# Performance work log

Hardware: AMD Instinct MI355X
Metric: run time of the kernel (lower is better)

Reference implementation:

```python
import jax, jax.numpy as jnp
import numpy as np

N, IN_DIM, OUT_DIM, HEADS = 8192, 256, 256, 2
C = OUT_DIM // HEADS  # per-head channel dim (concat=True)
ALPHA = 0.2
NEG = -9e15


def setup_inputs() -> dict:
    key = jax.random.key(0)
    ks = jax.random.split(key, 9)
    h = jax.random.normal(ks[0], (N, IN_DIM), dtype=jnp.float32)
    adj = jax.random.randint(ks[1], (N, N), 0, 2, dtype=jnp.int32)
    # torch nn.Linear weights are [out, in]; xavier-like scale
    def xav(k, shape):
        fan_in, fan_out = shape[1], shape[0]
        s = 1.414 * np.sqrt(6.0 / (fan_in + fan_out))
        return jax.random.uniform(k, shape, jnp.float32, -s, s)
    W1 = xav(ks[2], (HEADS * C, IN_DIM))
    W2 = xav(ks[3], (HEADS * C, IN_DIM))
    W3 = xav(ks[4], (HEADS * C, IN_DIM))
    b1 = jnp.zeros((HEADS * C,), jnp.float32)
    b2 = jnp.zeros((HEADS * C,), jnp.float32)
    b3 = jnp.zeros((HEADS * C,), jnp.float32)
    sa = 1.414 * np.sqrt(6.0 / (HEADS + 2 * C))
    a = jax.random.uniform(ks[5], (HEADS, 2 * C), jnp.float32, -sa, sa)
    return {"h": h, "adj": adj, "W1": W1, "b1": b1, "W2": W2, "b2": b2,
            "W3": W3, "b3": b3, "a": a}


def reference(h, adj, W1, b1, W2, b2, W3, b3, a):
    n = h.shape[0]
    W1h = (h @ W1.T + b1).reshape(n, HEADS, C)  # [N,H,C]
    W2h = (h @ W2.T + b2).reshape(n, HEADS, C)
    W3h = (h @ W3.T + b3).reshape(n, HEADS, C)
    # eij = a . [W1h_i || W2h_j] decomposes into per-node scores
    a1, a2 = a[:, :C], a[:, C:]
    s1 = jnp.einsum('nhc,hc->nh', W1h, a1)  # [N,H]
    s2 = jnp.einsum('nhc,hc->nh', W2h, a2)  # [N,H]
    e = jax.nn.leaky_relu(s1[:, None, :] + s2[None, :, :], ALPHA)  # [N,N,H]
    e = jnp.where(adj[:, :, None] == 1, e, NEG)
    att = jax.nn.softmax(e, axis=1)  # softmax over source dim j (dim=1)
    # dropout is identity in eval mode (training=False)
    h_prime = jnp.einsum('ijh,jhc->ihc', att, W3h)  # [N,H,C]
    return h_prime.reshape(n, HEADS * C)
```

## Files before the change

### kernel.cpp

```cpp
#include <hip/hip_runtime.h>
#include <hip/hip_bf16.h>

#define NN 8192
#define LOG2E 1.44269504088896f
#define S_SPLIT 8
#define JC 1024
#define NT 32

typedef __attribute__((ext_vector_type(8))) short short8;
typedef __attribute__((ext_vector_type(4))) float f32x4;
typedef __attribute__((ext_vector_type(4))) int int4v;

static __device__ __forceinline__ float bf2f(unsigned short u) {
    union { unsigned int i; float f; } v; v.i = ((unsigned int)u) << 16; return v.f;
}
static __device__ __forceinline__ unsigned short f2bf(float f) {
    union { float f; unsigned int i; } v; v.f = f;
    unsigned int lsb = (v.i >> 16) & 1u;
    v.i += 0x7fffu + lsb;
    return (unsigned short)(v.i >> 16);
}
static __device__ __forceinline__ unsigned int cvtpk(float lo, float hi) {
    unsigned int r;
    asm("v_cvt_pk_bf16_f32 %0, %1, %2" : "=v"(r) : "v"(lo), "v"(hi));
    return r;
}
static __device__ __forceinline__ float fexp2(float x) { return __builtin_amdgcn_exp2f(x); }

static __device__ __forceinline__ void cvt8(const float* __restrict__ p, short8& hi, short8& lo) {
    float4 u = *(const float4*)p;
    float4 v = *(const float4*)(p + 4);
    float f[8] = {u.x, u.y, u.z, u.w, v.x, v.y, v.z, v.w};
#pragma unroll
    for (int j = 0; j < 8; ++j) {
        unsigned short hb = f2bf(f[j]);
        hi[j] = (short)hb;
        lo[j] = (short)f2bf(f[j] - bf2f(hb));
    }
}

__global__ void prep_partial(const float* __restrict__ W1, const float* __restrict__ W2,
                             const float* __restrict__ a,
                             float* __restrict__ v1p, float* __restrict__ v2p) {
    int b = blockIdx.x;
    int t = threadIdx.x;
    int hh = t >> 8, k = t & 255;
    int c0 = (b & 7) * 16;
    const float* W = (b < 8) ? W1 : W2;
    int aoff = (b < 8) ? 0 : 128;
    float acc = 0.f;
    for (int c = c0; c < c0 + 16; ++c)
        acc += W[(size_t)(hh * 128 + c) * 256 + k] * a[hh * 256 + aoff + c];
    ((b < 8) ? v1p : v2p)[(b & 7) * 512 + t] = acc;
}

__global__ void prep_reduce(const float* __restrict__ b1, const float* __restrict__ b2,
                            const float* __restrict__ a,
                            const float* __restrict__ v1p, const float* __restrict__ v2p,
                            float* __restrict__ v1, float* __restrict__ v2, float* __restrict__ bd) {
    int t = threadIdx.x;
    float a1 = 0.f, a2 = 0.f;
    for (int b = 0; b < 8; ++b) { a1 += v1p[b * 512 + t]; a2 += v2p[b * 512 + t]; }
    v1[t] = a1;
    v2[t] = a2;
    int g = t >> 7;
    int hh = g >> 1, which = g & 1, c = t & 127;
    float prod = which ? b2[hh * 128 + c] * a[hh * 256 + 128 + c]
                       : b1[hh * 128 + c] * a[hh * 256 + c];
#pragma unroll
    for (int off = 1; off < 64; off <<= 1) prod += __shfl_xor(prod, off);
    __shared__ float ws[8];
    if ((t & 63) == 0) ws[t >> 6] = prod;
    __syncthreads();
    if (t < 4) bd[t] = ws[2 * t] + ws[2 * t + 1];
}

__global__ __launch_bounds__(256) void s_kernel(const float* __restrict__ hmat,
                         const float* __restrict__ v1, const float* __restrict__ v2,
                         const float* __restrict__ bd,
                         float* __restrict__ s1o, float* __restrict__ s2o) {
    int w = threadIdx.x >> 6, l = threadIdx.x & 63;
    int n = blockIdx.x * 4 + w;
    float4 hv  = *(const float4*)(hmat + (size_t)n * 256 + l * 4);
    float4 va0 = *(const float4*)(v1 + l * 4);
    float4 va1 = *(const float4*)(v1 + 256 + l * 4);
    float4 vb0 = *(const float4*)(v2 + l * 4);
    float4 vb1 = *(const float4*)(v2 + 256 + l * 4);
    float s10 = hv.x*va0.x + hv.y*va0.y + hv.z*va0.z + hv.w*va0.w;
    float s11 = hv.x*va1.x + hv.y*va1.y + hv.z*va1.z + hv.w*va1.w;
    float s20 = hv.x*vb0.x + hv.y*vb0.y + hv.z*vb0.z + hv.w*vb0.w;
    float s21 = hv.x*vb1.x + hv.y*vb1.y + hv.z*vb1.z + hv.w*vb1.w;
#pragma unroll
    for (int off = 1; off < 64; off <<= 1) {
        s10 += __shfl_xor(s10, off);
        s11 += __shfl_xor(s11, off);
        s20 += __shfl_xor(s20, off);
        s21 += __shfl_xor(s21, off);
    }
    if (l == 0) {
        s1o[n*2 + 0] = (s10 + bd[0]) * LOG2E;
        s1o[n*2 + 1] = (s11 + bd[2]) * LOG2E;
        s2o[n]       = (s20 + bd[1]) * LOG2E;
        s2o[NN + n]  = (s21 + bd[3]) * LOG2E;
    }
}

__global__ void wcvt_kernel(const float* __restrict__ W3,
                            unsigned short* __restrict__ w3hi, unsigned short* __restrict__ w3lo) {
    int i = blockIdx.x * 256 + threadIdx.x;
    float f = W3[i];
    unsigned short hb = f2bf(f);
    w3hi[i] = hb;
    w3lo[i] = f2bf(f - bf2f(hb));
}

__global__ __launch_bounds__(256) void w3_kernel(const float* __restrict__ hmat,
                                                 const unsigned short* __restrict__ w3hi,
                                                 const unsigned short* __restrict__ w3lo,
                                                 const float* __restrict__ b3,
                                                 unsigned short* __restrict__ w3b) {
    int tid = threadIdx.x;
    int w = tid >> 6, l = tid & 63;
    int m = l & 15, kq = l >> 4;
    int n0 = (blockIdx.x * 2 + (w & 1)) * 16;
    int c0 = (w >> 1) * 8;
    f32x4 acc[8];
#pragma unroll
    for (int ct = 0; ct < 8; ++ct) acc[ct] = (f32x4){0.f, 0.f, 0.f, 0.f};
    for (int k0 = 0; k0 < 256; k0 += 32) {
        short8 ahi, alo;
        cvt8(hmat + (size_t)(n0 + m) * 256 + k0 + kq * 8, ahi, alo);
#pragma unroll
        for (int ct = 0; ct < 8; ++ct) {
            int c = (c0 + ct) * 16 + m;
            short8 bhi = *(const short8*)&w3hi[(size_t)c * 256 + k0 + kq * 8];
            short8 blo = *(const short8*)&w3lo[(size_t)c * 256 + k0 + kq * 8];
            acc[ct] = __builtin_amdgcn_mfma_f32_16x16x32_bf16(ahi, bhi, acc[ct], 0, 0, 0);
            acc[ct] = __builtin_amdgcn_mfma_f32_16x16x32_bf16(alo, bhi, acc[ct], 0, 0, 0);
            acc[ct] = __builtin_amdgcn_mfma_f32_16x16x32_bf16(ahi, blo, acc[ct], 0, 0, 0);
        }
    }
#pragma unroll
    for (int ct = 0; ct < 8; ++ct) {
        int c = (c0 + ct) * 16 + m;
        float bias = b3[c];
#pragma unroll
        for (int e = 0; e < 4; ++e) {
            int n = n0 + kq * 4 + e;
            size_t idx = ((size_t)(n >> 5) * 16 + (c >> 4)) * 512 + (size_t)((((n >> 3) & 3) * 16 + m) * 8 + (n & 7));
            w3b[idx] = f2bf(acc[ct][e] + bias);
        }
    }
}

__global__ __launch_bounds__(512, 4) void attn_fused(
        const int* __restrict__ adj, const float* __restrict__ s1a,
        const float* __restrict__ s2h, const unsigned short* __restrict__ w3b,
        unsigned short* __restrict__ pacc, float* __restrict__ pden)
{
    __shared__ unsigned short Pt[2][2][64][32];
    __shared__ float s2t[2][JC];

    const int tid = threadIdx.x;
    const int wv = tid >> 6, ln = tid & 63;
    const int m = ln & 15, kq = ln >> 4;
    const int rg = wv & 1, cg = wv >> 1;
    const int hw = cg >> 1;
    const int r = tid >> 3, oct = tid & 7;
    const int i0 = blockIdx.x * 64;
    const int sidx = blockIdx.y;
    const int j0 = sidx * JC;
    const int sw = kq ^ ((m >> 1) & 3);

    const float s1r0 = s1a[(i0 + r) * 2 + 0];
    const float s1r1 = s1a[(i0 + r) * 2 + 1];
    const int* adjRow = adj + (size_t)(i0 + r) * NN + j0 + oct * 4;
    unsigned short* ptw = &Pt[0][0][0][0] + r * 32 + ((((oct >> 1) ^ ((r >> 1) & 3)) << 3) | ((oct & 1) << 2));
    const unsigned short* pta = &Pt[0][0][0][0] + (size_t)hw * 2048 + (rg * 32 + m) * 32 + (sw << 3);
    const unsigned short* w3p = w3b + ((size_t)(j0 >> 5) * 16 + cg * 4) * 512 + ln * 8;

    f32x4 acc[2][4];
    f32x4 accd[2];
#pragma unroll
    for (int rt = 0; rt < 2; ++rt) {
        accd[rt] = (f32x4){0.f, 0.f, 0.f, 0.f};
#pragma unroll
        for (int f = 0; f < 4; ++f) acc[rt][f] = (f32x4){0.f, 0.f, 0.f, 0.f};
    }
    short8 ones;
#pragma unroll
    for (int e = 0; e < 8; ++e) ones[e] = (short)0x3F80;

    for (int x = tid; x < 2 * JC; x += 512) {
        int h = x >> 10, j = x & (JC - 1);
        s2t[h][j] = s2h[(size_t)h * NN + j0 + j];
    }
    int4v aCur = __builtin_nontemporal_load((const int4v*)(adjRow));
    int4v aNxt = __builtin_nontemporal_load((const int4v*)(adjRow + 32));
    __syncthreads();

    for (int t = 0; t < NT; ++t) {
        const int buf = t & 1;
        const unsigned short* bp = w3p + (size_t)t * 8192;
        short8 bf0 = *(const short8*)(bp);
        short8 bf1 = *(const short8*)(bp + 512);
        short8 bf2 = *(const short8*)(bp + 1024);
        short8 bf3 = *(const short8*)(bp + 1536);
        int tn2 = (t + 2 < NT) ? t + 2 : NT - 1;
        int4v aNew = __builtin_nontemporal_load((const int4v*)(adjRow + tn2 * 32));
        {
            float4 sv0 = *(const float4*)&s2t[0][t * 32 + oct * 4];
            float4 sv1 = *(const float4*)&s2t[1][t * 32 + oct * 4];
            float x0, q0, q1, q2, q3, u0, u1, u2, u3;
            x0 = s1r0 + sv0.x; x0 = fmaxf(x0, 0.2f * x0); q0 = aCur.x ? fexp2(x0) : 0.f;
            x0 = s1r0 + sv0.y; x0 = fmaxf(x0, 0.2f * x0); q1 = aCur.y ? fexp2(x0) : 0.f;
            x0 = s1r0 + sv0.z; x0 = fmaxf(x0, 0.2f * x0); q2 = aCur.z ? fexp2(x0) : 0.f;
            x0 = s1r0 + sv0.w; x0 = fmaxf(x0, 0.2f * x0); q3 = aCur.w ? fexp2(x0) : 0.f;
            x0 = s1r1 + sv1.x; x0 = fmaxf(x0, 0.2f * x0); u0 = aCur.x ? fexp2(x0) : 0.f;
            x0 = s1r1 + sv1.y; x0 = fmaxf(x0, 0.2f * x0); u1 = aCur.y ? fexp2(x0) : 0.f;
            x0 = s1r1 + sv1.z; x0 = fmaxf(x0, 0.2f * x0); u2 = aCur.z ? fexp2(x0) : 0.f;
            x0 = s1r1 + sv1.w; x0 = fmaxf(x0, 0.2f * x0); u3 = aCur.w ? fexp2(x0) : 0.f;
            uint2 w0 = {cvtpk(q0, q1), cvtpk(q2, q3)};
            uint2 w1 = {cvtpk(u0, u1), cvtpk(u2, u3)};
            unsigned short* pw = ptw + buf * 4096;
            *(uint2*)pw = w0;
            *(uint2*)(pw + 2048) = w1;
        }
        asm volatile("s_waitcnt lgkmcnt(0)" ::: "memory");
        __builtin_amdgcn_sched_barrier(0);
        __builtin_amdgcn_s_barrier();
        asm volatile("" ::: "memory");
        {
            const unsigned short* pa = pta + buf * 4096;
            short8 a0 = *(const short8*)pa;
            short8 a1 = *(const short8*)(pa + 512);
            __builtin_amdgcn_s_setprio(1);
            acc[0][0] = __builtin_amdgcn_mfma_f32_16x16x32_bf16(a0, bf0, acc[0][0], 0, 0, 0);
            acc[1][0] = __builtin_amdgcn_mfma_f32_16x16x32_bf16(a1, bf0, acc[1][0], 0, 0, 0);
            acc[0][1] = __builtin_amdgcn_mfma_f32_16x16x32_bf16(a0, bf1, acc[0][1], 0, 0, 0);
            acc[1][1] = __builtin_amdgcn_mfma_f32_16x16x32_bf16(a1, bf1, acc[1][1], 0, 0, 0);
            acc[0][2] = __builtin_amdgcn_mfma_f32_16x16x32_bf16(a0, bf2, acc[0][2], 0, 0, 0);
            acc[1][2] = __builtin_amdgcn_mfma_f32_16x16x32_bf16(a1, bf2, acc[1][2], 0, 0, 0);
            acc[0][3] = __builtin_amdgcn_mfma_f32_16x16x32_bf16(a0, bf3, acc[0][3], 0, 0, 0);
            acc[1][3] = __builtin_amdgcn_mfma_f32_16x16x32_bf16(a1, bf3, acc[1][3], 0, 0, 0);
            if ((cg & 1) == 0) {
                accd[0] = __builtin_amdgcn_mfma_f32_16x16x32_bf16(a0, ones, accd[0], 0, 0, 0);
                accd[1] = __builtin_amdgcn_mfma_f32_16x16x32_bf16(a1, ones, accd[1], 0, 0, 0);
            }
            __builtin_amdgcn_s_setprio(0);
        }
        aCur = aNxt; aNxt = aNew;
    }

    if ((cg & 1) == 0 && m == 0) {
#pragma unroll
        for (int rt = 0; rt < 2; ++rt)
#pragma unroll
            for (int e = 0; e < 4; ++e) {
                int row = i0 + rg * 32 + rt * 16 + kq * 4 + e;
                pden[((size_t)sidx * NN + row) * 2 + hw] = accd[rt][e];
            }
    }
    size_t pb_ = (size_t)sidx * NN * 256;
#pragma unroll
    for (int rt = 0; rt < 2; ++rt)
#pragma unroll
        for (int e = 0; e < 4; ++e) {
            int row = i0 + rg * 32 + rt * 16 + kq * 4 + e;
#pragma unroll
            for (int f = 0; f < 4; ++f) {
                int col = cg * 64 + f * 16 + m;
                __builtin_nontemporal_store(f2bf(acc[rt][f][e]), &pacc[pb_ + (size_t)row * 256 + col]);
            }
        }
}

__global__ void combine_kernel(const unsigned short* __restrict__ pacc, const float* __restrict__ pden,
                               float* __restrict__ out) {
    size_t idx = ((size_t)blockIdx.x * 256 + threadIdx.x) * 8;
    int i = (int)(idx >> 8);
    int c = (int)(idx & 255);
    int hh = c >> 7;
    float acc[8];
#pragma unroll
    for (int e = 0; e < 8; ++e) acc[e] = 0.f;
    float den = 0.f;
    for (int s = 0; s < S_SPLIT; ++s) {
        uint4 v = *(const uint4*)&pacc[(size_t)s * NN * 256 + idx];
        unsigned int uu[4] = {v.x, v.y, v.z, v.w};
#pragma unroll
        for (int q = 0; q < 4; ++q) {
            acc[2*q]   += bf2f((unsigned short)(uu[q] & 0xffff));
            acc[2*q+1] += bf2f((unsigned short)(uu[q] >> 16));
        }
        den += pden[((size_t)s * NN + i) * 2 + hh];
    }
    float r = 1.f / den;
    float4 o0 = {acc[0]*r, acc[1]*r, acc[2]*r, acc[3]*r};
    float4 o1 = {acc[4]*r, acc[5]*r, acc[6]*r, acc[7]*r};
    *(float4*)&out[idx] = o0;
    *(float4*)&out[idx + 4] = o1;
}

extern "C" void kernel_launch(void* const* d_in, const int* in_sizes, int n_in,
                              void* d_out, int out_size, void* d_ws, size_t ws_size,
                              hipStream_t stream) {
    const float* hmat = (const float*)d_in[0];
    const int*   adj  = (const int*)d_in[1];
    const float* W1   = (const float*)d_in[2];
    const float* b1   = (const float*)d_in[3];
    const float* W2   = (const float*)d_in[4];
    const float* b2   = (const float*)d_in[5];
    const float* W3   = (const float*)d_in[6];
    const float* b3   = (const float*)d_in[7];
    const float* a    = (const float*)d_in[8];
    float* out = (float*)d_out;

    char* p = (char*)d_ws;
    float* v1   = (float*)p; p += 2048;
    float* v2   = (float*)p; p += 2048;
    float* bd   = (float*)p; p += 256;
    float* s1   = (float*)p; p += (size_t)NN * 2 * sizeof(float);
    float* s2h  = (float*)p; p += (size_t)NN * 2 * sizeof(float);
    float* v1p  = (float*)p; p += 8 * 512 * sizeof(float);
    float* v2p  = (float*)p; p += 8 * 512 * sizeof(float);
    unsigned short* w3hi = (unsigned short*)p; p += 65536 * 2;
    unsigned short* w3lo = (unsigned short*)p; p += 65536 * 2;
    unsigned short* w3b  = (unsigned short*)p; p += (size_t)NN * 256 * 2;
    float* pden = (float*)p; p += (size_t)S_SPLIT * NN * 2 * sizeof(float);
    unsigned short* pacc = (unsigned short*)p;

    prep_partial<<<16, 512, 0, stream>>>(W1, W2, a, v1p, v2p);
    prep_reduce<<<1, 512, 0, stream>>>(b1, b2, a, v1p, v2p, v1, v2, bd);
    s_kernel<<<NN / 4, 256, 0, stream>>>(hmat, v1, v2, bd, s1, s2h);
    wcvt_kernel<<<256, 256, 0, stream>>>(W3, w3hi, w3lo);
    w3_kernel<<<256, 256, 0, stream>>>(hmat, w3hi, w3lo, b3, w3b);
    attn_fused<<<dim3(NN / 64, S_SPLIT), 512, 0, stream>>>(adj, s1, s2h, w3b, pacc, pden);
    combine_kernel<<<(NN * 256) / (256 * 8), 256, 0, stream>>>(pacc, pden, out);
}
```

Measured before the change: 172.1 us.

## Pre-pack adjacency into bitmask and restructure attention to 256 threads

Adds a pre-pass that compresses the int32 adjacency matrix into one bit per entry. The attention kernel then stages these bits in shared memory instead of streaming int32 rows. The attention kernel drops to 4 waves per block, each computing all 64 rows, so it issues twice the MFMAs per wave with more accumulator registers. The softmax denominator moves from ones-vector MFMAs to scalar sums reduced with shuffles. Adjacency still has to be read in full once by the pack kernel, so the total traffic saving is small and an extra launch is added.

```diff
diff --git a/kernel.cpp b/kernel.cpp
--- a/kernel.cpp
+++ b/kernel.cpp
@@ -9,7 +9,6 @@
 
 typedef __attribute__((ext_vector_type(8))) short short8;
 typedef __attribute__((ext_vector_type(4))) float f32x4;
-typedef __attribute__((ext_vector_type(4))) int int4v;
 
 static __device__ __forceinline__ float bf2f(unsigned short u) {
     union { unsigned int i; float f; } v; v.i = ((unsigned int)u) << 16; return v.f;
@@ -37,6 +36,22 @@
         hi[j] = (short)hb;
         lo[j] = (short)f2bf(f[j] - bf2f(hb));
     }
+}
+
+__global__ __launch_bounds__(256) void pack_kernel(const int* __restrict__ adj,
+                                                   unsigned int* __restrict__ abits) {
+    int w = blockIdx.x * 256 + threadIdx.x;
+    const int* src = adj + (size_t)w * 32;
+    unsigned int bits = 0;
+#pragma unroll
+    for (int k = 0; k < 8; ++k) {
+        int4 v = *(const int4*)(src + k * 4);
+        bits |= (unsigned int)(v.x & 1) << (k * 4 + 0);
+        bits |= (unsigned int)(v.y & 1) << (k * 4 + 1);
+        bits |= (unsigned int)(v.z & 1) << (k * 4 + 2);
+        bits |= (unsigned int)(v.w & 1) << (k * 4 + 3);
+    }
+    abits[w] = bits;
 }
 
 __global__ void prep_partial(const float* __restrict__ W1, const float* __restrict__ W2,
@@ -153,20 +168,21 @@
     }
 }
 
-__global__ __launch_bounds__(512, 4) void attn_fused(
-        const int* __restrict__ adj, const float* __restrict__ s1a,
+__global__ __launch_bounds__(256, 4) void attn_fused(
+        const unsigned int* __restrict__ abits, const float* __restrict__ s1a,
         const float* __restrict__ s2h, const unsigned short* __restrict__ w3b,
         unsigned short* __restrict__ pacc, float* __restrict__ pden)
 {
     __shared__ unsigned short Pt[2][2][64][32];
     __shared__ float s2t[2][JC];
+    __shared__ unsigned int abt[64][32];
 
     const int tid = threadIdx.x;
-    const int wv = tid >> 6, ln = tid & 63;
+    const int ln = tid & 63;
     const int m = ln & 15, kq = ln >> 4;
-    const int rg = wv & 1, cg = wv >> 1;
+    const int cg = tid >> 6;
     const int hw = cg >> 1;
-    const int r = tid >> 3, oct = tid & 7;
+    const int r = tid >> 2, oc = tid & 3;
     const int i0 = blockIdx.x * 64;
     const int sidx = blockIdx.y;
     const int j0 = sidx * JC;
@@ -174,29 +190,25 @@
 
     const float s1r0 = s1a[(i0 + r) * 2 + 0];
     const float s1r1 = s1a[(i0 + r) * 2 + 1];
-    const int* adjRow = adj + (size_t)(i0 + r) * NN + j0 + oct * 4;
-    unsigned short* ptw = &Pt[0][0][0][0] + r * 32 + ((((oct >> 1) ^ ((r >> 1) & 3)) << 3) | ((oct & 1) << 2));
-    const unsigned short* pta = &Pt[0][0][0][0] + (size_t)hw * 2048 + (rg * 32 + m) * 32 + (sw << 3);
+    unsigned short* ptw = &Pt[0][0][0][0] + r * 32 + ((oc ^ ((r >> 1) & 3)) << 3);
+    const unsigned short* pta = &Pt[0][0][0][0] + hw * 2048 + m * 32 + (sw << 3);
     const unsigned short* w3p = w3b + ((size_t)(j0 >> 5) * 16 + cg * 4) * 512 + ln * 8;
 
-    f32x4 acc[2][4];
-    f32x4 accd[2];
-#pragma unroll
-    for (int rt = 0; rt < 2; ++rt) {
-        accd[rt] = (f32x4){0.f, 0.f, 0.f, 0.f};
+    f32x4 acc[4][4];
+#pragma unroll
+    for (int rt = 0; rt < 4; ++rt)
 #pragma unroll
         for (int f = 0; f < 4; ++f) acc[rt][f] = (f32x4){0.f, 0.f, 0.f, 0.f};
-    }
-    short8 ones;
-#pragma unroll
-    for (int e = 0; e < 8; ++e) ones[e] = (short)0x3F80;
-
-    for (int x = tid; x < 2 * JC; x += 512) {
+    float d0 = 0.f, d1 = 0.f;
+
+    for (int x = tid; x < 2 * JC; x += 256) {
         int h = x >> 10, j = x & (JC - 1);
         s2t[h][j] = s2h[(size_t)h * NN + j0 + j];
     }
-    int4v aCur = __builtin_nontemporal_load((const int4v*)(adjRow));
-    int4v aNxt = __builtin_nontemporal_load((const int4v*)(adjRow + 32));
+    for (int x = tid; x < 64 * 32; x += 256) {
+        int rr = x >> 5, tt = x & 31;
+        abt[rr][tt] = abits[(size_t)(i0 + rr) * 256 + (j0 >> 5) + tt];
+    }
     __syncthreads();
 
     for (int t = 0; t < NT; ++t) {
@@ -206,25 +218,30 @@
         short8 bf1 = *(const short8*)(bp + 512);
         short8 bf2 = *(const short8*)(bp + 1024);
         short8 bf3 = *(const short8*)(bp + 1536);
-        int tn2 = (t + 2 < NT) ? t + 2 : NT - 1;
-        int4v aNew = __builtin_nontemporal_load((const int4v*)(adjRow + tn2 * 32));
         {
-            float4 sv0 = *(const float4*)&s2t[0][t * 32 + oct * 4];
-            float4 sv1 = *(const float4*)&s2t[1][t * 32 + oct * 4];
-            float x0, q0, q1, q2, q3, u0, u1, u2, u3;
-            x0 = s1r0 + sv0.x; x0 = fmaxf(x0, 0.2f * x0); q0 = aCur.x ? fexp2(x0) : 0.f;
-            x0 = s1r0 + sv0.y; x0 = fmaxf(x0, 0.2f * x0); q1 = aCur.y ? fexp2(x0) : 0.f;
-            x0 = s1r0 + sv0.z; x0 = fmaxf(x0, 0.2f * x0); q2 = aCur.z ? fexp2(x0) : 0.f;
-            x0 = s1r0 + sv0.w; x0 = fmaxf(x0, 0.2f * x0); q3 = aCur.w ? fexp2(x0) : 0.f;
-            x0 = s1r1 + sv1.x; x0 = fmaxf(x0, 0.2f * x0); u0 = aCur.x ? fexp2(x0) : 0.f;
-            x0 = s1r1 + sv1.y; x0 = fmaxf(x0, 0.2f * x0); u1 = aCur.y ? fexp2(x0) : 0.f;
-            x0 = s1r1 + sv1.z; x0 = fmaxf(x0, 0.2f * x0); u2 = aCur.z ? fexp2(x0) : 0.f;
-            x0 = s1r1 + sv1.w; x0 = fmaxf(x0, 0.2f * x0); u3 = aCur.w ? fexp2(x0) : 0.f;
-            uint2 w0 = {cvtpk(q0, q1), cvtpk(q2, q3)};
-            uint2 w1 = {cvtpk(u0, u1), cvtpk(u2, u3)};
+            unsigned int bits = abt[r][t] >> (oc * 8);
+            float4 sv00 = *(const float4*)&s2t[0][t * 32 + oc * 8];
+            float4 sv01 = *(const float4*)&s2t[0][t * 32 + oc * 8 + 4];
+            float4 sv10 = *(const float4*)&s2t[1][t * 32 + oc * 8];
+            float4 sv11 = *(const float4*)&s2t[1][t * 32 + oc * 8 + 4];
+            float f0[8] = {sv00.x, sv00.y, sv00.z, sv00.w, sv01.x, sv01.y, sv01.z, sv01.w};
+            float f1[8] = {sv10.x, sv10.y, sv10.z, sv10.w, sv11.x, sv11.y, sv11.z, sv11.w};
+            float q[8], u[8];
+#pragma unroll
+            for (int k = 0; k < 8; ++k) {
+                float x0 = s1r0 + f0[k]; x0 = fmaxf(x0, 0.2f * x0);
+                float x1 = s1r1 + f1[k]; x1 = fmaxf(x1, 0.2f * x1);
+                bool on = (bits >> k) & 1u;
+                q[k] = on ? fexp2(x0) : 0.f;
+                u[k] = on ? fexp2(x1) : 0.f;
+            }
+            d0 += ((q[0] + q[1]) + (q[2] + q[3])) + ((q[4] + q[5]) + (q[6] + q[7]));
+            d1 += ((u[0] + u[1]) + (u[2] + u[3])) + ((u[4] + u[5]) + (u[6] + u[7]));
+            uint4 w0 = {cvtpk(q[0], q[1]), cvtpk(q[2], q[3]), cvtpk(q[4], q[5]), cvtpk(q[6], q[7])};
+            uint4 w1 = {cvtpk(u[0], u[1]), cvtpk(u[2], u[3]), cvtpk(u[4], u[5]), cvtpk(u[6], u[7])};
             unsigned short* pw = ptw + buf * 4096;
-            *(uint2*)pw = w0;
-            *(uint2*)(pw + 2048) = w1;
+            *(uint4*)pw = w0;
+            *(uint4*)(pw + 2048) = w1;
         }
         asm volatile("s_waitcnt lgkmcnt(0)" ::: "memory");
         __builtin_amdgcn_sched_barrier(0);
@@ -232,41 +249,44 @@
         asm volatile("" ::: "memory");
         {
             const unsigned short* pa = pta + buf * 4096;
-            short8 a0 = *(const short8*)pa;
+            short8 a0 = *(const short8*)(pa);
             short8 a1 = *(const short8*)(pa + 512);
+            short8 a2 = *(const short8*)(pa + 1024);
+            short8 a3 = *(const short8*)(pa + 1536);
             __builtin_amdgcn_s_setprio(1);
             acc[0][0] = __builtin_amdgcn_mfma_f32_16x16x32_bf16(a0, bf0, acc[0][0], 0, 0, 0);
             acc[1][0] = __builtin_amdgcn_mfma_f32_16x16x32_bf16(a1, bf0, acc[1][0], 0, 0, 0);
+            acc[2][0] = __builtin_amdgcn_mfma_f32_16x16x32_bf16(a2, bf0, acc[2][0], 0, 0, 0);
+            acc[3][0] = __builtin_amdgcn_mfma_f32_16x16x32_bf16(a3, bf0, acc[3][0], 0, 0, 0);
             acc[0][1] = __builtin_amdgcn_mfma_f32_16x16x32_bf16(a0, bf1, acc[0][1], 0, 0, 0);
             acc[1][1] = __builtin_amdgcn_mfma_f32_16x16x32_bf16(a1, bf1, acc[1][1], 0, 0, 0);
+            acc[2][1] = __builtin_amdgcn_mfma_f32_16x16x32_bf16(a2, bf1, acc[2][1], 0, 0, 0);
+            acc[3][1] = __builtin_amdgcn_mfma_f32_16x16x32_bf16(a3, bf1, acc[3][1], 0, 0, 0);
             acc[0][2] = __builtin_amdgcn_mfma_f32_16x16x32_bf16(a0, bf2, acc[0][2], 0, 0, 0);
             acc[1][2] = __builtin_amdgcn_mfma_f32_16x16x32_bf16(a1, bf2, acc[1][2], 0, 0, 0);
+            acc[2][2] = __builtin_amdgcn_mfma_f32_16x16x32_bf16(a2, bf2, acc[2][2], 0, 0, 0);
+            acc[3][2] = __builtin_amdgcn_mfma_f32_16x16x32_bf16(a3, bf2, acc[3][2], 0, 0, 0);
             acc[0][3] = __builtin_amdgcn_mfma_f32_16x16x32_bf16(a0, bf3, acc[0][3], 0, 0, 0);
             acc[1][3] = __builtin_amdgcn_mfma_f32_16x16x32_bf16(a1, bf3, acc[1][3], 0, 0, 0);
-            if ((cg & 1) == 0) {
-                accd[0] = __builtin_amdgcn_mfma_f32_16x16x32_bf16(a0, ones, accd[0], 0, 0, 0);
-                accd[1] = __builtin_amdgcn_mfma_f32_16x16x32_bf16(a1, ones, accd[1], 0, 0, 0);
-            }
+            acc[2][3] = __builtin_amdgcn_mfma_f32_16x16x32_bf16(a2, bf3, acc[2][3], 0, 0, 0);
+            acc[3][3] = __builtin_amdgcn_mfma_f32_16x16x32_bf16(a3, bf3, acc[3][3], 0, 0, 0);
             __builtin_amdgcn_s_setprio(0);
         }
-        aCur = aNxt; aNxt = aNew;
-    }
-
-    if ((cg & 1) == 0 && m == 0) {
-#pragma unroll
-        for (int rt = 0; rt < 2; ++rt)
-#pragma unroll
-            for (int e = 0; e < 4; ++e) {
-                int row = i0 + rg * 32 + rt * 16 + kq * 4 + e;
-                pden[((size_t)sidx * NN + row) * 2 + hw] = accd[rt][e];
-            }
+    }
+
+    d0 += __shfl_xor(d0, 1); d0 += __shfl_xor(d0, 2);
+    d1 += __shfl_xor(d1, 1); d1 += __shfl_xor(d1, 2);
+    if (oc == 0) {
+        size_t base = ((size_t)sidx * NN + i0 + r) * 2;
+        pden[base + 0] = d0;
+        pden[base + 1] = d1;
     }
     size_t pb_ = (size_t)sidx * NN * 256;
 #pragma unroll
-    for (int rt = 0; rt < 2; ++rt)
+    for (int rt = 0; rt < 4; ++rt)
 #pragma unroll
         for (int e = 0; e < 4; ++e) {
-            int row = i0 + rg * 32 + rt * 16 + kq * 4 + e;
+            int row = i0 + rt * 16 + kq * 4 + e;
 #pragma unroll
             for (int f = 0; f < 4; ++f) {
                 int col = cg * 64 + f * 16 + m;
@@ -327,14 +347,16 @@
     unsigned short* w3hi = (unsigned short*)p; p += 65536 * 2;
     unsigned short* w3lo = (unsigned short*)p; p += 65536 * 2;
     unsigned short* w3b  = (unsigned short*)p; p += (size_t)NN * 256 * 2;
+    unsigned int* abits  = (unsigned int*)p;   p += (size_t)NN * 256 * sizeof(unsigned int);
     float* pden = (float*)p; p += (size_t)S_SPLIT * NN * 2 * sizeof(float);
     unsigned short* pacc = (unsigned short*)p;
 
+    pack_kernel<<<(NN * 256) / 256, 256, 0, stream>>>(adj, abits);
     prep_partial<<<16, 512, 0, stream>>>(W1, W2, a, v1p, v2p);
     prep_reduce<<<1, 512, 0, stream>>>(b1, b2, a, v1p, v2p, v1, v2, bd);
     s_kernel<<<NN / 4, 256, 0, stream>>>(hmat, v1, v2, bd, s1, s2h);
     wcvt_kernel<<<256, 256, 0, stream>>>(W3, w3hi, w3lo);
     w3_kernel<<<256, 256, 0, stream>>>(hmat, w3hi, w3lo, b3, w3b);
-    attn_fused<<<dim3(NN / 64, S_SPLIT), 512, 0, stream>>>(adj, s1, s2h, w3b, pacc, pden);
+    attn_fused<<<dim3(NN / 64, S_SPLIT), 256, 0, stream>>>(abits, s1, s2h, w3b, pacc, pden);
     combine_kernel<<<(NN * 256) / (256 * 8), 256, 0, stream>>>(pacc, pden, out);
 }
```

After: 153.7 us. 10.7% less time.
